# Kernel optimization log

Hardware: AMD Instinct MI355X
Metric: run time of the kernel (lower is better)

Reference implementation:

```python
import jax, jax.numpy as jnp
import numpy as np

N, E, F_IN, H, EDIM, L, OUT = 100000, 1600000, 256, 128, 16, 3, 64


def setup_inputs() -> dict:
    key = jax.random.key(0)
    ks = jax.random.split(key, 12)
    s = lambda k, shape: jax.random.normal(k, shape, jnp.float32) * 0.05
    return dict(
        x=jax.random.normal(ks[0], (N, F_IN), jnp.float32),
        edge_index=jax.random.randint(ks[1], (2, E), 0, N, jnp.int32),
        edge_attr=jax.random.normal(ks[2], (E, EDIM), jnp.float32),
        in_w=s(ks[3], (F_IN, H)), in_b=jnp.zeros((H,), jnp.float32),
        Wk=s(ks[4], (L, H, H)), bk=jnp.zeros((L, H), jnp.float32),
        Wq=s(ks[5], (L, H, H)), bq=jnp.zeros((L, H), jnp.float32),
        Wv=s(ks[6], (L, H, H)), bv=jnp.zeros((L, H), jnp.float32),
        We=s(ks[7], (L, EDIM, H)), be=jnp.zeros((L, H), jnp.float32),
        Ws=s(ks[8], (L, H, H)), bs=jnp.zeros((L, H), jnp.float32),
        ln_g=jnp.ones((L, H), jnp.float32), ln_b=jnp.zeros((L, H), jnp.float32),
        out_w=s(ks[9], (H, OUT)),
    )


def _layernorm(x, g, b, eps=1e-5):
    mu = x.mean(-1, keepdims=True)
    var = ((x - mu) ** 2).mean(-1, keepdims=True)
    return (x - mu) * jax.lax.rsqrt(var + eps) * g + b


def reference(x, edge_index, edge_attr, in_w, in_b, Wk, bk, Wq, bq, Wv, bv,
              We, be, Ws, bs, ln_g, ln_b, out_w):
    src, dst = edge_index[0], edge_index[1]  # j (source), i (target)
    h = x @ in_w + in_b                      # in_proj; dropout_prob=0 -> identity
    n = h.shape[0]
    n_layers = Wk.shape[0]
    for l in range(n_layers):
        # ResGatedGraphConv: out_i = W_skip x_i + sum_j sigmoid(k_i + e_ij + q_j) * v_j
        k = h @ Wk[l] + bk[l]                # keys on targets  [N,H]
        q = h @ Wq[l] + bq[l]                # queries on sources [N,H]
        v = h @ Wv[l] + bv[l]                # values on sources [N,H]
        e = edge_attr @ We[l] + be[l]        # edge embedding [E,H]
        gate = jax.nn.sigmoid(k[dst] + e + q[src])   # [E,H]
        msg = gate * v[src]                  # [E,H]
        agg = jax.ops.segment_sum(msg, dst, num_segments=n)  # scatter-add [N,H]
        h = agg + (h @ Ws[l] + bs[l])        # root/skip term
        h = jax.nn.gelu(_layernorm(h, ln_g[l], ln_b[l]), approximate=False)
    return h @ out_w                          # out_proj (bias=False)
```

## Files before the change

### kernel.cpp

```cpp
#include <hip/hip_runtime.h>
#include <hip/hip_fp16.h>
#include <cmath>

#define Nn   100000
#define Ee   1600000
#define FIN  256
#define Hh   128
#define EDIMM 16
#define NL   3
#define NOUT 64
#define LOG2E 1.4426950408889634f

typedef _Float16 f16x8 __attribute__((ext_vector_type(8)));
typedef float f32x4 __attribute__((ext_vector_type(4)));

static __device__ __forceinline__ __half2 u2h2(unsigned int u) {
  union { unsigned int u; __half2 h; } c; c.u = u; return c.h;
}
static __device__ __forceinline__ unsigned int h22u(__half2 h) {
  union { unsigned int u; __half2 h; } c; c.h = h; return c.u;
}

#define PK_FMA_LO(acc, a, w) \
  asm("v_pk_fma_f16 %0, %1, %2, %0 op_sel:[0,0,0] op_sel_hi:[0,1,1]" \
      : "+v"(acc) : "v"(a), "v"(w))
#define PK_FMA_HI(acc, a, w) \
  asm("v_pk_fma_f16 %0, %1, %2, %0 op_sel:[1,0,0] op_sel_hi:[1,1,1]" \
      : "+v"(acc) : "v"(a), "v"(w))

__global__ __launch_bounds__(256) void prep_inw_kernel(const float* __restrict__ in_w,
    __half* __restrict__ in_wT) {
  int i = blockIdx.x * 256 + threadIdx.x;
  if (i < FIN * Hh) {
    int k = i >> 7, n = i & 127;
    in_wT[(size_t)n * FIN + k] = __float2half(in_w[i]);
  }
}

__global__ __launch_bounds__(256) void in_proj_mfma_kernel(const float* __restrict__ x,
    const __half* __restrict__ in_wT, const float* __restrict__ b, __half* __restrict__ h) {
  __shared__ __half Wl[128][136];
  __shared__ __half Ht[32][136];
  int r0 = blockIdx.x * 32;
  int tid = threadIdx.x;
  int wv = tid >> 6, lane = tid & 63;
  int rowHalf = wv & 1, colHalf = wv >> 1;
  int quad = lane >> 4, l16 = lane & 15;

  f32x4 acc[4];
#pragma unroll
  for (int t = 0; t < 4; t++) acc[t] = (f32x4){0.f, 0.f, 0.f, 0.f};

  for (int ph = 0; ph < 2; ph++) {
    for (int i = tid; i < 2048; i += 256) {
      int rw = i >> 4, cw = i & 15;
      *(uint4*)(&Wl[rw][cw * 8]) =
          *(const uint4*)(in_wT + (size_t)rw * FIN + ph * 128 + cw * 8);
    }
    for (int i = tid; i < 1024; i += 256) {
      int r = i >> 5, c4 = i & 31;
      float4 f = *(const float4*)(x + (size_t)(r0 + r) * FIN + ph * 128 + c4 * 4);
      *(uint2*)(&Ht[r][c4 * 4]) =
          make_uint2(h22u(__floats2half2_rn(f.x, f.y)), h22u(__floats2half2_rn(f.z, f.w)));
    }
    __syncthreads();
#pragma unroll
    for (int kstep = 0; kstep < 4; kstep++) {
      f16x8 afrag = *(const f16x8*)(&Ht[rowHalf * 16 + l16][kstep * 32 + quad * 8]);
#pragma unroll
      for (int t = 0; t < 4; t++) {
        int n = colHalf * 64 + t * 16 + l16;
        f16x8 bfrag = *(const f16x8*)(&Wl[n][kstep * 32 + quad * 8]);
        acc[t] = __builtin_amdgcn_mfma_f32_16x16x32_f16(afrag, bfrag, acc[t], 0, 0, 0);
      }
    }
    __syncthreads();
  }

#pragma unroll
  for (int t = 0; t < 4; t++) {
    int col = colHalf * 64 + t * 16 + l16;
    float bval = b[col];
#pragma unroll
    for (int r = 0; r < 4; r++) {
      int row = r0 + rowHalf * 16 + quad * 4 + r;
      h[(size_t)row * Hh + col] = __float2half(acc[t][r] + bval);
    }
  }
}

__global__ __launch_bounds__(256) void prep_weights_kernel(const float* __restrict__ Wk,
    const float* __restrict__ Wq, const float* __restrict__ Wv, const float* __restrict__ Ws,
    __half* __restrict__ WtT) {
  int mat = blockIdx.x, l = blockIdx.y;
  const float* W = (mat == 0 ? Wk : mat == 1 ? Wq : mat == 2 ? Wv : Ws) + (size_t)l * Hh * Hh;
  float sc = (mat < 2) ? LOG2E : 1.f;
  __half* out = WtT + ((size_t)(l * 4 + mat)) * Hh * Hh;
  for (int i = threadIdx.x; i < Hh * Hh; i += 256) {
    int k = i >> 7, n = i & 127;
    out[(size_t)n * Hh + k] = __float2half(W[i] * sc);
  }
}

__global__ __launch_bounds__(256) void kqvs_mfma_kernel(
    const __half* __restrict__ h, const __half* __restrict__ WtT_l,
    const float* __restrict__ bk, const float* __restrict__ bq,
    const float* __restrict__ bv, const float* __restrict__ bs,
    __half* __restrict__ kb, __half* __restrict__ qvj, __half* __restrict__ hnew) {
  __shared__ __half Wl[128][136];
  __shared__ __half Ht[32][136];
  int mat = blockIdx.x;
  int r0 = blockIdx.y * 32;
  int tid = threadIdx.x;

  const uint4* wg = (const uint4*)(WtT_l + (size_t)mat * Hh * Hh);
  for (int i = tid; i < 2048; i += 256) {
    int rw = i >> 4, cw = i & 15;
    *(uint4*)(&Wl[rw][cw * 8]) = wg[i];
  }
  const uint4* hg = (const uint4*)(h + (size_t)r0 * Hh);
  for (int i = tid; i < 512; i += 256) {
    int rh = i >> 4, ch = i & 15;
    *(uint4*)(&Ht[rh][ch * 8]) = hg[i];
  }
  __syncthreads();

  int wv = tid >> 6, lane = tid & 63;
  int rowHalf = wv & 1, colHalf = wv >> 1;
  int quad = lane >> 4, l16 = lane & 15;

  f32x4 acc[4];
#pragma unroll
  for (int t = 0; t < 4; t++) acc[t] = (f32x4){0.f, 0.f, 0.f, 0.f};

#pragma unroll
  for (int kstep = 0; kstep < 4; kstep++) {
    f16x8 afrag = *(const f16x8*)(&Ht[rowHalf * 16 + l16][kstep * 32 + quad * 8]);
#pragma unroll
    for (int t = 0; t < 4; t++) {
      int n = colHalf * 64 + t * 16 + l16;
      f16x8 bfrag = *(const f16x8*)(&Wl[n][kstep * 32 + quad * 8]);
      acc[t] = __builtin_amdgcn_mfma_f32_16x16x32_f16(afrag, bfrag, acc[t], 0, 0, 0);
    }
  }

  const float* bp = (mat == 0) ? bk : (mat == 1) ? bq : (mat == 2) ? bv : bs;
  float bscale = (mat < 2) ? LOG2E : 1.f;
#pragma unroll
  for (int t = 0; t < 4; t++) {
    int col = colHalf * 64 + t * 16 + l16;
    float bval = bp[col] * bscale;
#pragma unroll
    for (int r = 0; r < 4; r++) {
      int row = r0 + rowHalf * 16 + quad * 4 + r;
      __half hv = __float2half(acc[t][r] + bval);
      if (mat == 0)       kb[(size_t)row * Hh + col] = hv;
      else if (mat == 1)  qvj[(size_t)row * 256 + (col >> 1) * 4 + (col & 1)] = hv;
      else if (mat == 2)  qvj[(size_t)row * 256 + (col >> 1) * 4 + 2 + (col & 1)] = hv;
      else                hnew[(size_t)row * Hh + col] = hv;
    }
  }
}

__global__ __launch_bounds__(256) void zero_kernel(int* __restrict__ p, int n) {
  int i = blockIdx.x * 256 + threadIdx.x;
  if (i < n) p[i] = 0;
}

__global__ __launch_bounds__(256) void hist_kernel(const int* __restrict__ ei_dst,
                                                   int* __restrict__ counts) {
  int e = blockIdx.x * 256 + threadIdx.x;
  if (e < Ee) atomicAdd(&counts[ei_dst[e]], 1);
}

__global__ __launch_bounds__(256) void scan_block_kernel(const int* __restrict__ counts,
    int* __restrict__ rowptr, int* __restrict__ bsums) {
  __shared__ int tsums[256];
  int b = blockIdx.x, t = threadIdx.x;
  int base = b * 1024 + t * 4;
  int v[4]; int s = 0;
#pragma unroll
  for (int j = 0; j < 4; j++) {
    int idx = base + j;
    v[j] = (idx < Nn) ? counts[idx] : 0;
    s += v[j];
  }
  tsums[t] = s;
  __syncthreads();
  for (int off = 1; off < 256; off <<= 1) {
    int y = (t >= off) ? tsums[t - off] : 0;
    __syncthreads();
    tsums[t] += y;
    __syncthreads();
  }
  int excl = tsums[t] - s;
#pragma unroll
  for (int j = 0; j < 4; j++) {
    int idx = base + j;
    if (idx < Nn) rowptr[idx] = excl;
    excl += v[j];
  }
  if (t == 255) bsums[b] = tsums[255];
}

__global__ __launch_bounds__(128) void scan_sums_kernel(int* __restrict__ bsums, int nb) {
  __shared__ int sh[128];
  int t = threadIdx.x;
  int v = (t < nb) ? bsums[t] : 0;
  sh[t] = v;
  __syncthreads();
  for (int off = 1; off < 128; off <<= 1) {
    int y = (t >= off) ? sh[t - off] : 0;
    __syncthreads();
    sh[t] += y;
    __syncthreads();
  }
  if (t < nb) bsums[t] = sh[t] - v;
}

__global__ __launch_bounds__(256) void finalize_rowptr_kernel(int* __restrict__ rowptr,
    const int* __restrict__ bsums, int* __restrict__ cursor) {
  int i = blockIdx.x * 256 + threadIdx.x;
  if (i < Nn) {
    int r = rowptr[i] + bsums[i >> 10];
    rowptr[i] = r;
    cursor[i] = r;
  }
  if (i == Nn) rowptr[Nn] = Ee;
}

__global__ __launch_bounds__(256) void fill_perm_kernel(const int* __restrict__ ei_src,
    const int* __restrict__ ei_dst, const float* __restrict__ ea,
    int* __restrict__ cursor, int* __restrict__ src_perm,
    unsigned int* __restrict__ ea_perm) {
  int e = blockIdx.x * 256 + threadIdx.x;
  if (e < Ee) {
    int d = ei_dst[e];
    int slot = atomicAdd(&cursor[d], 1);
    src_perm[slot] = ei_src[e];
    const float4* s = (const float4*)(ea + (size_t)e * EDIMM);
    float4 f0 = s[0], f1 = s[1], f2 = s[2], f3 = s[3];
    uint4* dp = (uint4*)(ea_perm + (size_t)slot * 8);
    dp[0] = make_uint4(h22u(__floats2half2_rn(f0.x, f0.y)), h22u(__floats2half2_rn(f0.z, f0.w)),
                       h22u(__floats2half2_rn(f1.x, f1.y)), h22u(__floats2half2_rn(f1.z, f1.w)));
    dp[1] = make_uint4(h22u(__floats2half2_rn(f2.x, f2.y)), h22u(__floats2half2_rn(f2.z, f2.w)),
                       h22u(__floats2half2_rn(f3.x, f3.y)), h22u(__floats2half2_rn(f3.z, f3.w)));
  }
}

#define EA_CAP 48
__global__ __launch_bounds__(256, 6) void edge_csr_kernel(
    const __half* __restrict__ kb, const __half* __restrict__ qvj,
    const int* __restrict__ src_perm, const unsigned int* __restrict__ ea_perm,
    const int* __restrict__ rowptr,
    const float* __restrict__ We_l, const float* __restrict__ be_l,
    const float* __restrict__ ln_g_l, const float* __restrict__ ln_b_l,
    __half* __restrict__ hbuf) {
  __shared__ uint4 lds_ea[4][EA_CAP * 2];
  int wave = threadIdx.x >> 6;
  int lane = threadIdx.x & 63;
  int row = blockIdx.x * 4 + wave;
  int c0 = lane * 2;

  unsigned wpk[EDIMM];
#pragma unroll
  for (int d = 0; d < EDIMM; d++) {
    float2 wv = *(const float2*)(We_l + d * Hh + c0);
    wpk[d] = h22u(__floats2half2_rn(wv.x * LOG2E, wv.y * LOG2E));
  }
  float2 bef = *(const float2*)(be_l + c0);
  __half2 bev = __floats2half2_rn(bef.x * LOG2E, bef.y * LOG2E);

  __half2 kpk = *(const __half2*)(kb + (size_t)row * Hh + c0);
  unsigned kbev_u = h22u(__hadd2(kpk, bev));

  float agg0 = 0.f, agg1 = 0.f;
  int beg = rowptr[row], end = rowptr[row + 1];
  int deg = end - beg;
  int nl = (deg < EA_CAP) ? deg : EA_CAP;

  char* lbase = (char*)&lds_ea[wave][0];
  {
    int row_bytes = nl << 5;
    const char* gsrc = (const char*)(ea_perm + (size_t)beg * 8);
    for (int c = 0; c < row_bytes; c += 1024) {
      int o = c + lane * 16;
      if (o < row_bytes) {
        __builtin_amdgcn_global_load_lds(
            (__attribute__((address_space(1))) void*)(gsrc + o),
            (__attribute__((address_space(3))) void*)(lbase + c),
            16, 0, 0);
      }
    }
  }

  const char* qvb = (const char*)qvj;
  unsigned loff = (unsigned)(lane << 3);

  auto edge_math = [&](uint4 eA, uint4 eB, uint2 qv) {
    unsigned acc = kbev_u;
    PK_FMA_LO(acc, eA.x, wpk[0]);  PK_FMA_HI(acc, eA.x, wpk[1]);
    PK_FMA_LO(acc, eA.y, wpk[2]);  PK_FMA_HI(acc, eA.y, wpk[3]);
    PK_FMA_LO(acc, eA.z, wpk[4]);  PK_FMA_HI(acc, eA.z, wpk[5]);
    PK_FMA_LO(acc, eA.w, wpk[6]);  PK_FMA_HI(acc, eA.w, wpk[7]);
    PK_FMA_LO(acc, eB.x, wpk[8]);  PK_FMA_HI(acc, eB.x, wpk[9]);
    PK_FMA_LO(acc, eB.y, wpk[10]); PK_FMA_HI(acc, eB.y, wpk[11]);
    PK_FMA_LO(acc, eB.z, wpk[12]); PK_FMA_HI(acc, eB.z, wpk[13]);
    PK_FMA_LO(acc, eB.w, wpk[14]); PK_FMA_HI(acc, eB.w, wpk[15]);
    __half2 pre = __hadd2(u2h2(acc), u2h2(qv.x));
    float p0 = __half2float(__low2half(pre));
    float p1 = __half2float(__high2half(pre));
    float ex0, ex1;
    asm("v_exp_f32 %0, -%1" : "=v"(ex0) : "v"(p0));
    asm("v_exp_f32 %0, -%1" : "=v"(ex1) : "v"(p1));
    float g0 = __builtin_amdgcn_rcpf(1.f + ex0);
    float g1 = __builtin_amdgcn_rcpf(1.f + ex1);
    __half2 vh = u2h2(qv.y);
    agg0 += g0 * __half2float(__low2half(vh));
    agg1 += g1 * __half2float(__high2half(vh));
  };

  {
    int nf = nl & ~3;
    int e = 0;
    uint2 qA0, qA1, qA2, qA3;
    if (nf) {
      int4 s4 = *(const int4*)(src_perm + beg);
      qA0 = *(const uint2*)(qvb + (((unsigned)s4.x << 9) + loff));
      qA1 = *(const uint2*)(qvb + (((unsigned)s4.y << 9) + loff));
      qA2 = *(const uint2*)(qvb + (((unsigned)s4.z << 9) + loff));
      qA3 = *(const uint2*)(qvb + (((unsigned)s4.w << 9) + loff));
    }
    asm volatile("s_waitcnt vmcnt(0)" ::: "memory");

    for (; e + 8 <= nf; e += 4) {
      int4 s4n = *(const int4*)(src_perm + beg + e + 4);
      uint2 qB0 = *(const uint2*)(qvb + (((unsigned)s4n.x << 9) + loff));
      uint2 qB1 = *(const uint2*)(qvb + (((unsigned)s4n.y << 9) + loff));
      uint2 qB2 = *(const uint2*)(qvb + (((unsigned)s4n.z << 9) + loff));
      uint2 qB3 = *(const uint2*)(qvb + (((unsigned)s4n.w << 9) + loff));
      const uint4* ee = (const uint4*)(lbase + (e << 5));
      edge_math(ee[0], ee[1], qA0);
      edge_math(ee[2], ee[3], qA1);
      edge_math(ee[4], ee[5], qA2);
      edge_math(ee[6], ee[7], qA3);
      qA0 = qB0; qA1 = qB1; qA2 = qB2; qA3 = qB3;
    }
    if (nf) {
      const uint4* ee = (const uint4*)(lbase + (e << 5));
      edge_math(ee[0], ee[1], qA0);
      edge_math(ee[2], ee[3], qA1);
      edge_math(ee[4], ee[5], qA2);
      edge_math(ee[6], ee[7], qA3);
      e += 4;
    }
    for (; e < nl; e++) {
      int src = src_perm[beg + e];
      uint2 qv = *(const uint2*)(qvb + (((unsigned)src << 9) + loff));
      const uint4* ee = (const uint4*)(lbase + (e << 5));
      edge_math(ee[0], ee[1], qv);
    }
    for (int eg = beg + nl; eg < end; eg++) {
      int src = src_perm[eg];
      const uint4* eb = (const uint4*)(ea_perm + (size_t)eg * 8);
      uint4 a0 = eb[0], a1 = eb[1];
      uint2 qv = *(const uint2*)(qvb + (((unsigned)src << 9) + loff));
      edge_math(a0, a1, qv);
    }
  }

  __half2 hv2 = *(const __half2*)(hbuf + (size_t)row * Hh + c0);
  float y0 = __half2float(hv2.x) + agg0, y1 = __half2float(hv2.y) + agg1;
  float s = y0 + y1;
#pragma unroll
  for (int off = 32; off; off >>= 1) s += __shfl_xor(s, off);
  float mu = s * (1.f / 128.f);
  float d0 = y0 - mu, d1 = y1 - mu;
  float vv = d0 * d0 + d1 * d1;
#pragma unroll
  for (int off = 32; off; off >>= 1) vv += __shfl_xor(vv, off);
  float rstd = rsqrtf(vv * (1.f / 128.f) + 1e-5f);
  float2 lg = *(const float2*)(ln_g_l + c0);
  float2 lb = *(const float2*)(ln_b_l + c0);
  float o0 = d0 * rstd * lg.x + lb.x;
  float o1 = d1 * rstd * lg.y + lb.y;
  o0 = 0.5f * o0 * (1.f + erff(o0 * 0.70710678118654752f));
  o1 = 0.5f * o1 * (1.f + erff(o1 * 0.70710678118654752f));
  *(__half2*)(hbuf + (size_t)row * Hh + c0) = __floats2half2_rn(o0, o1);
}

__global__ __launch_bounds__(64) void out_proj_kernel(const __half* __restrict__ h,
    const float* __restrict__ w, float* __restrict__ out) {
  __shared__ float hs[16][Hh];
  int r0 = blockIdx.x * 16;
  const uint4* hg = (const uint4*)(h + (size_t)r0 * Hh);
  for (int i = threadIdx.x; i < 256; i += 64) {
    uint4 u = hg[i];
    int r = i >> 4, c = (i & 15) * 8;
    __half2 ha = u2h2(u.x), hb = u2h2(u.y), hc = u2h2(u.z), hd = u2h2(u.w);
    hs[r][c+0] = __half2float(ha.x); hs[r][c+1] = __half2float(ha.y);
    hs[r][c+2] = __half2float(hb.x); hs[r][c+3] = __half2float(hb.y);
    hs[r][c+4] = __half2float(hc.x); hs[r][c+5] = __half2float(hc.y);
    hs[r][c+6] = __half2float(hd.x); hs[r][c+7] = __half2float(hd.y);
  }
  __syncthreads();
  int t = threadIdx.x;
  float acc[16] = {};
  for (int kk = 0; kk < Hh; kk++) {
    float wv = w[kk * NOUT + t];
#pragma unroll
    for (int r = 0; r < 16; r++) acc[r] += hs[r][kk] * wv;
  }
#pragma unroll
  for (int r = 0; r < 16; r++) out[(size_t)(r0 + r) * NOUT + t] = acc[r];
}

extern "C" void kernel_launch(void* const* d_in, const int* in_sizes, int n_in,
                              void* d_out, int out_size, void* d_ws, size_t ws_size,
                              hipStream_t stream) {
  const float* x    = (const float*)d_in[0];
  const int*   ei   = (const int*)d_in[1];
  const float* ea   = (const float*)d_in[2];
  const float* in_w = (const float*)d_in[3];
  const float* in_b = (const float*)d_in[4];
  const float* Wk   = (const float*)d_in[5];
  const float* bk   = (const float*)d_in[6];
  const float* Wq   = (const float*)d_in[7];
  const float* bq   = (const float*)d_in[8];
  const float* Wv   = (const float*)d_in[9];
  const float* bv   = (const float*)d_in[10];
  const float* We   = (const float*)d_in[11];
  const float* be   = (const float*)d_in[12];
  const float* Ws   = (const float*)d_in[13];
  const float* bs   = (const float*)d_in[14];
  const float* ln_g = (const float*)d_in[15];
  const float* ln_b = (const float*)d_in[16];
  const float* out_w = (const float*)d_in[17];
  float* out = (float*)d_out;

  const int* ei_src = ei;
  const int* ei_dst = ei + Ee;

  size_t NH = (size_t)Nn * Hh;
  char* wsp = (char*)d_ws;
  __half* hA = (__half*)wsp;          wsp += NH * 2;
  __half* hB = (__half*)wsp;          wsp += NH * 2;
  __half* kb = (__half*)wsp;          wsp += NH * 2;
  __half* qvj = (__half*)wsp;         wsp += NH * 2 * 2;
  __half* WtT = (__half*)wsp;         wsp += (size_t)NL * 4 * Hh * Hh * 2;
  __half* in_wT = (__half*)wsp;       wsp += (size_t)FIN * Hh * 2;
  int* rowptr = (int*)wsp;            wsp += (Nn + 1) * 4;
  int* cursor = (int*)wsp;            wsp += Nn * 4;
  int* bsums  = (int*)wsp;            wsp += 128 * 4;
  int* src_perm = (int*)wsp;          wsp += (size_t)Ee * 4;
  unsigned int* ea_perm = (unsigned int*)wsp; wsp += (size_t)Ee * 32;

  const int NB_SCAN = (Nn + 1023) / 1024;

  zero_kernel<<<(Nn + 255) / 256, 256, 0, stream>>>(cursor, Nn);
  hist_kernel<<<(Ee + 255) / 256, 256, 0, stream>>>(ei_dst, cursor);
  scan_block_kernel<<<NB_SCAN, 256, 0, stream>>>(cursor, rowptr, bsums);
  scan_sums_kernel<<<1, 128, 0, stream>>>(bsums, NB_SCAN);
  finalize_rowptr_kernel<<<(Nn + 1 + 255) / 256, 256, 0, stream>>>(rowptr, bsums, cursor);
  fill_perm_kernel<<<(Ee + 255) / 256, 256, 0, stream>>>(ei_src, ei_dst, ea, cursor,
                                                         src_perm, ea_perm);
  prep_weights_kernel<<<dim3(4, NL), 256, 0, stream>>>(Wk, Wq, Wv, Ws, WtT);
  prep_inw_kernel<<<(FIN * Hh + 255) / 256, 256, 0, stream>>>(in_w, in_wT);

  in_proj_mfma_kernel<<<Nn / 32, 256, 0, stream>>>(x, in_wT, in_b, hA);

  __half* h  = hA;
  __half* hn = hB;
  for (int l = 0; l < NL; l++) {
    kqvs_mfma_kernel<<<dim3(4, Nn / 32), 256, 0, stream>>>(h,
        WtT + (size_t)l * 4 * Hh * Hh,
        bk + l * Hh, bq + l * Hh, bv + l * Hh, bs + l * Hh,
        kb, qvj, hn);
    edge_csr_kernel<<<Nn / 4, 256, 0, stream>>>(kb, qvj, src_perm, ea_perm,
        rowptr, We + l * EDIMM * Hh, be + l * Hh,
        ln_g + l * Hh, ln_b + l * Hh, hn);
    __half* tmp = h; h = hn; hn = tmp;
  }

  out_proj_kernel<<<Nn / 16, 64, 0, stream>>>(h, out_w, out);
}
```

Measured before the change: 1.181 ms.

## Loop four weight matrices per block in KQVS and process four rows per wave in edge kernel

```diff
diff --git a/kernel.cpp b/kernel.cpp
--- a/kernel.cpp
+++ b/kernel.cpp
@@ -109,56 +109,73 @@
     __half* __restrict__ kb, __half* __restrict__ qvj, __half* __restrict__ hnew) {
   __shared__ __half Wl[128][136];
   __shared__ __half Ht[32][136];
-  int mat = blockIdx.x;
-  int r0 = blockIdx.y * 32;
+  int r0 = blockIdx.x * 32;
   int tid = threadIdx.x;
 
-  const uint4* wg = (const uint4*)(WtT_l + (size_t)mat * Hh * Hh);
-  for (int i = tid; i < 2048; i += 256) {
-    int rw = i >> 4, cw = i & 15;
-    *(uint4*)(&Wl[rw][cw * 8]) = wg[i];
-  }
   const uint4* hg = (const uint4*)(h + (size_t)r0 * Hh);
-  for (int i = tid; i < 512; i += 256) {
-    int rh = i >> 4, ch = i & 15;
-    *(uint4*)(&Ht[rh][ch * 8]) = hg[i];
-  }
-  __syncthreads();
+  uint4 h0 = hg[tid], h1 = hg[tid + 256];
+  const uint4* wg0 = (const uint4*)(WtT_l);
+  uint4 wreg[8];
+#pragma unroll
+  for (int j = 0; j < 8; j++) wreg[j] = wg0[tid + 256 * j];
+  {
+    int rh = tid >> 4, ch = tid & 15;
+    *(uint4*)(&Ht[rh][ch * 8]) = h0;
+    int i2 = tid + 256;
+    rh = i2 >> 4; ch = i2 & 15;
+    *(uint4*)(&Ht[rh][ch * 8]) = h1;
+  }
 
   int wv = tid >> 6, lane = tid & 63;
   int rowHalf = wv & 1, colHalf = wv >> 1;
   int quad = lane >> 4, l16 = lane & 15;
 
-  f32x4 acc[4];
-#pragma unroll
-  for (int t = 0; t < 4; t++) acc[t] = (f32x4){0.f, 0.f, 0.f, 0.f};
-
-#pragma unroll
-  for (int kstep = 0; kstep < 4; kstep++) {
-    f16x8 afrag = *(const f16x8*)(&Ht[rowHalf * 16 + l16][kstep * 32 + quad * 8]);
+#pragma unroll 1
+  for (int mat = 0; mat < 4; mat++) {
+#pragma unroll
+    for (int j = 0; j < 8; j++) {
+      int i = tid + 256 * j;
+      int rw = i >> 4, cw = i & 15;
+      *(uint4*)(&Wl[rw][cw * 8]) = wreg[j];
+    }
+    __syncthreads();
+    if (mat < 3) {
+      const uint4* wgn = (const uint4*)(WtT_l + (size_t)(mat + 1) * Hh * Hh);
+#pragma unroll
+      for (int j = 0; j < 8; j++) wreg[j] = wgn[tid + 256 * j];
+    }
+
+    f32x4 acc[4];
+#pragma unroll
+    for (int t = 0; t < 4; t++) acc[t] = (f32x4){0.f, 0.f, 0.f, 0.f};
+#pragma unroll
+    for (int kstep = 0; kstep < 4; kstep++) {
+      f16x8 afrag = *(const f16x8*)(&Ht[rowHalf * 16 + l16][kstep * 32 + quad * 8]);
+#pragma unroll
+      for (int t = 0; t < 4; t++) {
+        int n = colHalf * 64 + t * 16 + l16;
+        f16x8 bfrag = *(const f16x8*)(&Wl[n][kstep * 32 + quad * 8]);
+        acc[t] = __builtin_amdgcn_mfma_f32_16x16x32_f16(afrag, bfrag, acc[t], 0, 0, 0);
+      }
+    }
+
+    const float* bp = (mat == 0) ? bk : (mat == 1) ? bq : (mat == 2) ? bv : bs;
+    float bscale = (mat < 2) ? LOG2E : 1.f;
 #pragma unroll
     for (int t = 0; t < 4; t++) {
-      int n = colHalf * 64 + t * 16 + l16;
-      f16x8 bfrag = *(const f16x8*)(&Wl[n][kstep * 32 + quad * 8]);
-      acc[t] = __builtin_amdgcn_mfma_f32_16x16x32_f16(afrag, bfrag, acc[t], 0, 0, 0);
-    }
-  }
-
-  const float* bp = (mat == 0) ? bk : (mat == 1) ? bq : (mat == 2) ? bv : bs;
-  float bscale = (mat < 2) ? LOG2E : 1.f;
-#pragma unroll
-  for (int t = 0; t < 4; t++) {
-    int col = colHalf * 64 + t * 16 + l16;
-    float bval = bp[col] * bscale;
-#pragma unroll
-    for (int r = 0; r < 4; r++) {
-      int row = r0 + rowHalf * 16 + quad * 4 + r;
-      __half hv = __float2half(acc[t][r] + bval);
-      if (mat == 0)       kb[(size_t)row * Hh + col] = hv;
-      else if (mat == 1)  qvj[(size_t)row * 256 + (col >> 1) * 4 + (col & 1)] = hv;
-      else if (mat == 2)  qvj[(size_t)row * 256 + (col >> 1) * 4 + 2 + (col & 1)] = hv;
-      else                hnew[(size_t)row * Hh + col] = hv;
-    }
+      int col = colHalf * 64 + t * 16 + l16;
+      float bval = bp[col] * bscale;
+#pragma unroll
+      for (int r = 0; r < 4; r++) {
+        int row = r0 + rowHalf * 16 + quad * 4 + r;
+        __half hv = __float2half(acc[t][r] + bval);
+        if (mat == 0)       kb[(size_t)row * Hh + col] = hv;
+        else if (mat == 1)  qvj[(size_t)row * 256 + (col >> 1) * 4 + (col & 1)] = hv;
+        else if (mat == 2)  qvj[(size_t)row * 256 + (col >> 1) * 4 + 2 + (col & 1)] = hv;
+        else                hnew[(size_t)row * Hh + col] = hv;
+      }
+    }
+    __syncthreads();
   }
 }
 
@@ -248,7 +265,7 @@
   }
 }
 
-#define EA_CAP 48
+#define EA_CAP4 160
 __global__ __launch_bounds__(256, 6) void edge_csr_kernel(
     const __half* __restrict__ kb, const __half* __restrict__ qvj,
     const int* __restrict__ src_perm, const unsigned int* __restrict__ ea_perm,
@@ -256,10 +273,10 @@
     const float* __restrict__ We_l, const float* __restrict__ be_l,
     const float* __restrict__ ln_g_l, const float* __restrict__ ln_b_l,
     __half* __restrict__ hbuf) {
-  __shared__ uint4 lds_ea[4][EA_CAP * 2];
+  __shared__ uint4 lds_ea[4][EA_CAP4 * 2];
   int wave = threadIdx.x >> 6;
   int lane = threadIdx.x & 63;
-  int row = blockIdx.x * 4 + wave;
+  int r0 = (blockIdx.x * 4 + wave) * 4;
   int c0 = lane * 2;
 
   unsigned wpk[EDIMM];
@@ -271,18 +288,21 @@
   float2 bef = *(const float2*)(be_l + c0);
   __half2 bev = __floats2half2_rn(bef.x * LOG2E, bef.y * LOG2E);
 
-  __half2 kpk = *(const __half2*)(kb + (size_t)row * Hh + c0);
-  unsigned kbev_u = h22u(__hadd2(kpk, bev));
-
-  float agg0 = 0.f, agg1 = 0.f;
-  int beg = rowptr[row], end = rowptr[row + 1];
-  int deg = end - beg;
-  int nl = (deg < EA_CAP) ? deg : EA_CAP;
+  int4 rp4 = *(const int4*)(rowptr + r0);
+  int rp[5] = {rp4.x, rp4.y, rp4.z, rp4.w, rowptr[r0 + 4]};
+
+  unsigned kbev_u[4];
+#pragma unroll
+  for (int ri = 0; ri < 4; ri++)
+    kbev_u[ri] = h22u(__hadd2(*(const __half2*)(kb + (size_t)(r0 + ri) * Hh + c0), bev));
+
+  int nl = rp[4] - rp[0];
+  if (nl > EA_CAP4) nl = EA_CAP4;
 
   char* lbase = (char*)&lds_ea[wave][0];
   {
     int row_bytes = nl << 5;
-    const char* gsrc = (const char*)(ea_perm + (size_t)beg * 8);
+    const char* gsrc = (const char*)(ea_perm + (size_t)rp[0] * 8);
     for (int c = 0; c < row_bytes; c += 1024) {
       int o = c + lane * 16;
       if (o < row_bytes) {
@@ -296,36 +316,46 @@
 
   const char* qvb = (const char*)qvj;
   unsigned loff = (unsigned)(lane << 3);
-
-  auto edge_math = [&](uint4 eA, uint4 eB, uint2 qv) {
-    unsigned acc = kbev_u;
-    PK_FMA_LO(acc, eA.x, wpk[0]);  PK_FMA_HI(acc, eA.x, wpk[1]);
-    PK_FMA_LO(acc, eA.y, wpk[2]);  PK_FMA_HI(acc, eA.y, wpk[3]);
-    PK_FMA_LO(acc, eA.z, wpk[4]);  PK_FMA_HI(acc, eA.z, wpk[5]);
-    PK_FMA_LO(acc, eA.w, wpk[6]);  PK_FMA_HI(acc, eA.w, wpk[7]);
-    PK_FMA_LO(acc, eB.x, wpk[8]);  PK_FMA_HI(acc, eB.x, wpk[9]);
-    PK_FMA_LO(acc, eB.y, wpk[10]); PK_FMA_HI(acc, eB.y, wpk[11]);
-    PK_FMA_LO(acc, eB.z, wpk[12]); PK_FMA_HI(acc, eB.z, wpk[13]);
-    PK_FMA_LO(acc, eB.w, wpk[14]); PK_FMA_HI(acc, eB.w, wpk[15]);
-    __half2 pre = __hadd2(u2h2(acc), u2h2(qv.x));
-    float p0 = __half2float(__low2half(pre));
-    float p1 = __half2float(__high2half(pre));
-    float ex0, ex1;
-    asm("v_exp_f32 %0, -%1" : "=v"(ex0) : "v"(p0));
-    asm("v_exp_f32 %0, -%1" : "=v"(ex1) : "v"(p1));
-    float g0 = __builtin_amdgcn_rcpf(1.f + ex0);
-    float g1 = __builtin_amdgcn_rcpf(1.f + ex1);
-    __half2 vh = u2h2(qv.y);
-    agg0 += g0 * __half2float(__low2half(vh));
-    agg1 += g1 * __half2float(__high2half(vh));
-  };
-
-  {
-    int nf = nl & ~3;
-    int e = 0;
+  const int* spb = src_perm + rp[0];
+
+#pragma unroll
+  for (int ri = 0; ri < 4; ri++) {
+    unsigned kb_u = kbev_u[ri];
+    float agg0 = 0.f, agg1 = 0.f;
+    int ls = rp[ri] - rp[0];
+    int le = rp[ri + 1] - rp[0];
+    int lend = le < nl ? le : nl;
+    if (lend < ls) lend = ls;
+
+    auto edge_math = [&](uint4 eA, uint4 eB, uint2 qv) {
+      unsigned acc = kb_u;
+      PK_FMA_LO(acc, eA.x, wpk[0]);  PK_FMA_HI(acc, eA.x, wpk[1]);
+      PK_FMA_LO(acc, eA.y, wpk[2]);  PK_FMA_HI(acc, eA.y, wpk[3]);
+      PK_FMA_LO(acc, eA.z, wpk[4]);  PK_FMA_HI(acc, eA.z, wpk[5]);
+      PK_FMA_LO(acc, eA.w, wpk[6]);  PK_FMA_HI(acc, eA.w, wpk[7]);
+      PK_FMA_LO(acc, eB.x, wpk[8]);  PK_FMA_HI(acc, eB.x, wpk[9]);
+      PK_FMA_LO(acc, eB.y, wpk[10]); PK_FMA_HI(acc, eB.y, wpk[11]);
+      PK_FMA_LO(acc, eB.z, wpk[12]); PK_FMA_HI(acc, eB.z, wpk[13]);
+      PK_FMA_LO(acc, eB.w, wpk[14]); PK_FMA_HI(acc, eB.w, wpk[15]);
+      __half2 pre = __hadd2(u2h2(acc), u2h2(qv.x));
+      float p0 = __half2float(__low2half(pre));
+      float p1 = __half2float(__high2half(pre));
+      float ex0, ex1;
+      asm("v_exp_f32 %0, -%1" : "=v"(ex0) : "v"(p0));
+      asm("v_exp_f32 %0, -%1" : "=v"(ex1) : "v"(p1));
+      float g0 = __builtin_amdgcn_rcpf(1.f + ex0);
+      float g1 = __builtin_amdgcn_rcpf(1.f + ex1);
+      __half2 vh = u2h2(qv.y);
+      agg0 += g0 * __half2float(__low2half(vh));
+      agg1 += g1 * __half2float(__high2half(vh));
+    };
+
+    int e = ls;
+    int nfull = (lend - e) & ~3;
+    int nfe = e + nfull;
     uint2 qA0, qA1, qA2, qA3;
-    if (nf) {
-      int4 s4 = *(const int4*)(src_perm + beg);
+    if (nfull) {
+      int4 s4 = *(const int4*)(spb + e);
       qA0 = *(const uint2*)(qvb + (((unsigned)s4.x << 9) + loff));
       qA1 = *(const uint2*)(qvb + (((unsigned)s4.y << 9) + loff));
       qA2 = *(const uint2*)(qvb + (((unsigned)s4.z << 9) + loff));
@@ -333,8 +363,8 @@
     }
     asm volatile("s_waitcnt vmcnt(0)" ::: "memory");
 
-    for (; e + 8 <= nf; e += 4) {
-      int4 s4n = *(const int4*)(src_perm + beg + e + 4);
+    for (; e + 8 <= nfe; e += 4) {
+      int4 s4n = *(const int4*)(spb + e + 4);
       uint2 qB0 = *(const uint2*)(qvb + (((unsigned)s4n.x << 9) + loff));
       uint2 qB1 = *(const uint2*)(qvb + (((unsigned)s4n.y << 9) + loff));
       uint2 qB2 = *(const uint2*)(qvb + (((unsigned)s4n.z << 9) + loff));
@@ -346,7 +376,7 @@
       edge_math(ee[6], ee[7], qA3);
       qA0 = qB0; qA1 = qB1; qA2 = qB2; qA3 = qB3;
     }
-    if (nf) {
+    if (nfull) {
       const uint4* ee = (const uint4*)(lbase + (e << 5));
       edge_math(ee[0], ee[1], qA0);
       edge_math(ee[2], ee[3], qA1);
@@ -354,39 +384,40 @@
       edge_math(ee[6], ee[7], qA3);
       e += 4;
     }
-    for (; e < nl; e++) {
-      int src = src_perm[beg + e];
+    for (; e < lend; e++) {
+      int src = spb[e];
       uint2 qv = *(const uint2*)(qvb + (((unsigned)src << 9) + loff));
       const uint4* ee = (const uint4*)(lbase + (e << 5));
       edge_math(ee[0], ee[1], qv);
     }
-    for (int eg = beg + nl; eg < end; eg++) {
+    for (int eg = rp[0] + lend; eg < rp[ri + 1]; eg++) {
       int src = src_perm[eg];
       const uint4* eb = (const uint4*)(ea_perm + (size_t)eg * 8);
       uint4 a0 = eb[0], a1 = eb[1];
       uint2 qv = *(const uint2*)(qvb + (((unsigned)src << 9) + loff));
       edge_math(a0, a1, qv);
     }
-  }
-
-  __half2 hv2 = *(const __half2*)(hbuf + (size_t)row * Hh + c0);
-  float y0 = __half2float(hv2.x) + agg0, y1 = __half2float(hv2.y) + agg1;
-  float s = y0 + y1;
-#pragma unroll
-  for (int off = 32; off; off >>= 1) s += __shfl_xor(s, off);
-  float mu = s * (1.f / 128.f);
-  float d0 = y0 - mu, d1 = y1 - mu;
-  float vv = d0 * d0 + d1 * d1;
-#pragma unroll
-  for (int off = 32; off; off >>= 1) vv += __shfl_xor(vv, off);
-  float rstd = rsqrtf(vv * (1.f / 128.f) + 1e-5f);
-  float2 lg = *(const float2*)(ln_g_l + c0);
-  float2 lb = *(const float2*)(ln_b_l + c0);
-  float o0 = d0 * rstd * lg.x + lb.x;
-  float o1 = d1 * rstd * lg.y + lb.y;
-  o0 = 0.5f * o0 * (1.f + erff(o0 * 0.70710678118654752f));
-  o1 = 0.5f * o1 * (1.f + erff(o1 * 0.70710678118654752f));
-  *(__half2*)(hbuf + (size_t)row * Hh + c0) = __floats2half2_rn(o0, o1);
+
+    int row = r0 + ri;
+    __half2 hv2 = *(const __half2*)(hbuf + (size_t)row * Hh + c0);
+    float y0 = __half2float(hv2.x) + agg0, y1 = __half2float(hv2.y) + agg1;
+    float s = y0 + y1;
+#pragma unroll
+    for (int off = 32; off; off >>= 1) s += __shfl_xor(s, off);
+    float mu = s * (1.f / 128.f);
+    float d0 = y0 - mu, d1 = y1 - mu;
+    float vv = d0 * d0 + d1 * d1;
+#pragma unroll
+    for (int off = 32; off; off >>= 1) vv += __shfl_xor(vv, off);
+    float rstd = rsqrtf(vv * (1.f / 128.f) + 1e-5f);
+    float2 lg = *(const float2*)(ln_g_l + c0);
+    float2 lb = *(const float2*)(ln_b_l + c0);
+    float o0 = d0 * rstd * lg.x + lb.x;
+    float o1 = d1 * rstd * lg.y + lb.y;
+    o0 = 0.5f * o0 * (1.f + erff(o0 * 0.70710678118654752f));
+    o1 = 0.5f * o1 * (1.f + erff(o1 * 0.70710678118654752f));
+    *(__half2*)(hbuf + (size_t)row * Hh + c0) = __floats2half2_rn(o0, o1);
+  }
 }
 
 __global__ __launch_bounds__(64) void out_proj_kernel(const __half* __restrict__ h,
@@ -472,11 +503,11 @@
   __half* h  = hA;
   __half* hn = hB;
   for (int l = 0; l < NL; l++) {
-    kqvs_mfma_kernel<<<dim3(4, Nn / 32), 256, 0, stream>>>(h,
+    kqvs_mfma_kernel<<<Nn / 32, 256, 0, stream>>>(h,
         WtT + (size_t)l * 4 * Hh * Hh,
         bk + l * Hh, bq + l * Hh, bv + l * Hh, bs + l * Hh,
         kb, qvj, hn);
-    edge_csr_kernel<<<Nn / 4, 256, 0, stream>>>(kb, qvj, src_perm, ea_perm,
+    edge_csr_kernel<<<Nn / 16, 256, 0, stream>>>(kb, qvj, src_perm, ea_perm,
         rowptr, We + l * EDIMM * Hh, be + l * Hh,
         ln_g + l * Hh, ln_b + l * Hh, hn);
     __half* tmp = h; h = hn; hn = tmp;
```

New measurement: 1.446 ms. +22.4%, slower.
